# Performance work log

Hardware: AMD Instinct MI355X
Metric: run time of the kernel (lower is better)

## Reference

```python
import jax, jax.numpy as jnp
import numpy as np

HEAD_SIZE = 128
NEG_INF = -1000000000.0

def setup_inputs() -> dict:
    key = jax.random.key(0)
    k1, k2, k3, k4 = jax.random.split(key, 4)
    B, T, C = 8, 2048, 1024
    x = jax.random.normal(k1, (B, T, C), dtype=jnp.float32)
    Wq = jax.random.normal(k2, (C, HEAD_SIZE), dtype=jnp.float32) * (1.0 / np.sqrt(C))
    Wk = jax.random.normal(k3, (C, HEAD_SIZE), dtype=jnp.float32) * (1.0 / np.sqrt(C))
    Wv = jax.random.normal(k4, (C, HEAD_SIZE), dtype=jnp.float32) * (1.0 / np.sqrt(C))
    return {"x": x, "Wq": Wq, "Wk": Wk, "Wv": Wv}

def reference(x, Wq, Wk, Wv):
    # x: [B, T, C]; projections: [B, T, H]
    T = x.shape[1]
    q = jnp.einsum('btc,ch->bth', x, Wq)
    k = jnp.einsum('btc,ch->bth', x, Wk)
    v = jnp.einsum('btc,ch->bth', x, Wv)
    scale = 1.0 / jnp.sqrt(jnp.float32(HEAD_SIZE))
    wei = jnp.einsum('bth,bsh->bts', q, k) * scale  # [B, T, T]
    causal = jnp.tril(jnp.ones((T, T), dtype=bool))
    wei = jnp.where(causal, wei, NEG_INF)
    wei = jax.nn.softmax(wei, axis=-1)
    # dropout is identity (deterministic=True)
    out = jnp.einsum('bts,bsh->bth', wei, v)  # [B, T, H]
    return out
```

## Files before the change

### kernel.cpp

```cpp
#include <hip/hip_runtime.h>
#include <hip/hip_bf16.h>
#include <stdint.h>

#define B_ 8
#define T_ 2048
#define C_ 1024
#define H_ 128
#define BT (B_*T_)
#define SCALE 0.08838834764831845f
#define CH 8

typedef __attribute__((ext_vector_type(8))) short bf16x8;
typedef __attribute__((ext_vector_type(4))) float f32x4;

__device__ __forceinline__ ushort f2bf(float f) {
  union { float f; uint32_t u; } un; un.f = f;
  return (ushort)((un.u + 0x7fffu + ((un.u >> 16) & 1u)) >> 16);
}
__device__ __forceinline__ float bf2f(ushort h) {
  union { uint32_t u; float f; } un; un.u = ((uint32_t)h) << 16;
  return un.f;
}

__global__ __launch_bounds__(256) void wtrans_kernel(
    const float* __restrict__ Wq, const float* __restrict__ Wk,
    const float* __restrict__ Wv, ushort* __restrict__ wt)
{
  const int tt = blockIdx.x * 256 + threadIdx.x;
  const int n = tt >> 6;
  const int k0 = (tt & 63) << 4;
  const float* W = (n < 128) ? Wq : (n < 256 ? Wk : Wv);
  const int h = n & 127;
  ushort tmp[16];
  #pragma unroll
  for (int j = 0; j < 16; ++j)
    tmp[j] = f2bf(W[(size_t)(k0 + j) * H_ + h]);
  *reinterpret_cast<bf16x8*>(&wt[(size_t)n * C_ + k0]) =
      *reinterpret_cast<bf16x8*>(&tmp[0]);
  *reinterpret_cast<bf16x8*>(&wt[(size_t)n * C_ + k0 + 8]) =
      *reinterpret_cast<bf16x8*>(&tmp[8]);
}

__global__ __launch_bounds__(256, 3) void proj_kernel(
    const float* __restrict__ x, const ushort* __restrict__ wt,
    ushort* __restrict__ qh, ushort* __restrict__ kh, ushort* __restrict__ vt)
{
  __shared__ __align__(16) ushort As[64][64];
  __shared__ __align__(16) ushort Bs[128][64];
  const int tid  = threadIdx.x;
  const int lane = tid & 63, wave = tid >> 6;
  const int l15  = lane & 15, l4 = lane >> 4;
  const int o  = (blockIdx.x & 7) * 96 + (blockIdx.x >> 3);
  const int mb = o / 3, nb = o - mb * 3;
  const int m0 = mb * 64, n0 = nb * 128;
  const int wr = wave >> 1, wc = wave & 1;

  f32x4 acc[2][4];
  #pragma unroll
  for (int i = 0; i < 2; ++i)
    #pragma unroll
    for (int j = 0; j < 4; ++j) acc[i][j] = f32x4{0.f, 0.f, 0.f, 0.f};

  for (int k0 = 0; k0 < C_; k0 += 64) {
    __syncthreads();
    #pragma unroll
    for (int it = 0; it < 4; ++it) {
      const int f4 = it * 256 + tid;
      const int r = f4 >> 4, c4 = f4 & 15;
      float4 v = *reinterpret_cast<const float4*>(
          &x[(size_t)(m0 + r) * C_ + k0 + 4 * c4]);
      ushort4 pk;
      pk.x = f2bf(v.x); pk.y = f2bf(v.y); pk.z = f2bf(v.z); pk.w = f2bf(v.w);
      const int ch = (c4 >> 1) ^ (r & 7);
      *reinterpret_cast<ushort4*>(&As[r][ch * 8 + (c4 & 1) * 4]) = pk;
    }
    #pragma unroll
    for (int it = 0; it < 4; ++it) {
      const int f8 = it * 256 + tid;
      const int r = f8 >> 3, c8 = f8 & 7;
      const int ch = c8 ^ (r & 7);
      *reinterpret_cast<bf16x8*>(&Bs[r][ch * 8]) =
          *reinterpret_cast<const bf16x8*>(
              &wt[(size_t)(n0 + r) * C_ + k0 + c8 * 8]);
    }
    __syncthreads();

    bf16x8 a[2][2], b[4][2];
    #pragma unroll
    for (int mi = 0; mi < 2; ++mi)
      #pragma unroll
      for (int kc = 0; kc < 2; ++kc) {
        const int row = wr * 32 + mi * 16 + l15;
        const int ch = (kc * 4 + l4) ^ (row & 7);
        a[mi][kc] = *reinterpret_cast<const bf16x8*>(&As[row][ch * 8]);
      }
    #pragma unroll
    for (int ni = 0; ni < 4; ++ni)
      #pragma unroll
      for (int kc = 0; kc < 2; ++kc) {
        const int row = wc * 64 + ni * 16 + l15;
        const int ch = (kc * 4 + l4) ^ (row & 7);
        b[ni][kc] = *reinterpret_cast<const bf16x8*>(&Bs[row][ch * 8]);
      }

    __builtin_amdgcn_s_setprio(1);
    if (nb != 2) {
      #pragma unroll
      for (int mi = 0; mi < 2; ++mi)
        #pragma unroll
        for (int ni = 0; ni < 4; ++ni)
          #pragma unroll
          for (int kc = 0; kc < 2; ++kc)
            acc[mi][ni] = __builtin_amdgcn_mfma_f32_16x16x32_bf16(
                a[mi][kc], b[ni][kc], acc[mi][ni], 0, 0, 0);
    } else {
      #pragma unroll
      for (int mi = 0; mi < 2; ++mi)
        #pragma unroll
        for (int ni = 0; ni < 4; ++ni)
          #pragma unroll
          for (int kc = 0; kc < 2; ++kc)
            acc[mi][ni] = __builtin_amdgcn_mfma_f32_16x16x32_bf16(
                b[ni][kc], a[mi][kc], acc[mi][ni], 0, 0, 0);
    }
    __builtin_amdgcn_s_setprio(0);
  }

  if (nb != 2) {
    ushort* dst = (nb == 0) ? qh : kh;
    #pragma unroll
    for (int mi = 0; mi < 2; ++mi)
      #pragma unroll
      for (int ni = 0; ni < 4; ++ni)
        #pragma unroll
        for (int reg = 0; reg < 4; ++reg) {
          const int row = m0 + wr * 32 + mi * 16 + l4 * 4 + reg;
          const int col = wc * 64 + ni * 16 + l15;
          dst[(size_t)row * H_ + col] = f2bf(acc[mi][ni][reg]);
        }
  } else {
    #pragma unroll
    for (int mi = 0; mi < 2; ++mi)
      #pragma unroll
      for (int ni = 0; ni < 4; ++ni)
        #pragma unroll
        for (int reg = 0; reg < 4; ++reg) {
          const int h = wc * 64 + ni * 16 + l4 * 4 + reg;
          const int gr = m0 + wr * 32 + mi * 16 + l15;
          const int b = gr >> 11, t = gr & 2047;
          vt[((size_t)b * H_ + h) * T_ + t] = f2bf(acc[mi][ni][reg]);
        }
  }
}

__global__ __launch_bounds__(256) void attn_kernel(
    const ushort* __restrict__ qh, const ushort* __restrict__ kh,
    const ushort* __restrict__ vt, ushort* __restrict__ pO,
    float* __restrict__ pm, float* __restrict__ pl, float* __restrict__ out)
{
  __shared__ __align__(16) ushort Ks[64][128];
  __shared__ __align__(16) ushort Vs[128][64];
  __shared__ __align__(16) ushort Ps[4][16][64];
  const int tid  = threadIdx.x;
  const int lane = tid & 63, wave = tid >> 6;
  const int l15  = lane & 15, l4 = lane >> 4;
  const int o = (blockIdx.x & 7) * 80 + (blockIdx.x >> 3);
  const int b = o / 80, u = o % 80;
  int g = 0;
  if (u >= 8)  g = 1;
  if (u >= 24) g = 2;
  if (u >= 48) g = 3;
  const int gp1 = g + 1;
  const int u2 = u - 4 * g * gp1;
  const int qi = 8 * g + u2 / gp1;
  const int ci = u2 % gp1;
  const int nchunk = gp1;
  const int q0 = qi * 64;
  const int kt0 = ci * CH;
  const int kt1 = min(qi + 1, kt0 + CH);
  const size_t mbase = (size_t)b * T_ + q0;
  const int swz = l15 & 7;

  bf16x8 qa[4];
  {
    const ushort* qrow = &qh[(mbase + wave * 16 + l15) * H_];
    #pragma unroll
    for (int kc = 0; kc < 4; ++kc)
      qa[kc] = *reinterpret_cast<const bf16x8*>(&qrow[kc * 32 + l4 * 8]);
  }

  f32x4 o_[8];
  #pragma unroll
  for (int i = 0; i < 8; ++i) o_[i] = f32x4{0.f, 0.f, 0.f, 0.f};
  float mrow[4] = {-1e9f, -1e9f, -1e9f, -1e9f};
  float lrow[4] = {0.f, 0.f, 0.f, 0.f};

  for (int kt = kt0; kt < kt1; ++kt) {
    const int kv0 = kt * 64;
    __syncthreads();
    for (int i = tid; i < 1024; i += 256) {
      const int r = i >> 4, c8 = i & 15;
      const int c8s = (c8 & 7) ^ (r & 7);
      *reinterpret_cast<bf16x8*>(&Ks[r][((c8 & 8) | c8s) * 8]) =
          *reinterpret_cast<const bf16x8*>(
              &kh[((size_t)b * T_ + kv0 + r) * H_ + c8 * 8]);
    }
    for (int i = tid; i < 1024; i += 256) {
      const int r = i >> 3, c8 = i & 7;
      const int c8s = c8 ^ (r & 7);
      *reinterpret_cast<bf16x8*>(&Vs[r][c8s * 8]) =
          *reinterpret_cast<const bf16x8*>(
              &vt[((size_t)b * H_ + r) * T_ + kv0 + c8 * 8]);
    }
    __syncthreads();

    f32x4 s[4];
    __builtin_amdgcn_s_setprio(1);
    #pragma unroll
    for (int ct = 0; ct < 4; ++ct) {
      s[ct] = f32x4{0.f, 0.f, 0.f, 0.f};
      #pragma unroll
      for (int kc = 0; kc < 4; ++kc) {
        const int chunk = ((kc * 4 + l4) & 7) ^ swz;
        bf16x8 kb = *reinterpret_cast<const bf16x8*>(
            &Ks[ct * 16 + l15][(((kc * 4 + l4) & 8) | chunk) * 8]);
        s[ct] = __builtin_amdgcn_mfma_f32_16x16x32_bf16(qa[kc], kb, s[ct], 0, 0, 0);
      }
    }
    __builtin_amdgcn_s_setprio(0);

    const bool diag = (kv0 == q0);
    float sv[4][4];
    #pragma unroll
    for (int ct = 0; ct < 4; ++ct)
      #pragma unroll
      for (int reg = 0; reg < 4; ++reg) {
        float v = s[ct][reg] * SCALE;
        if (diag) {
          const int sg = kv0 + ct * 16 + l15;
          const int rg = q0 + wave * 16 + l4 * 4 + reg;
          if (sg > rg) v = -1e9f;
        }
        sv[ct][reg] = v;
      }
    float mnew[4], alpha[4], ls[4];
    #pragma unroll
    for (int reg = 0; reg < 4; ++reg) {
      float m = fmaxf(fmaxf(sv[0][reg], sv[1][reg]), fmaxf(sv[2][reg], sv[3][reg]));
      #pragma unroll
      for (int msk = 1; msk < 16; msk <<= 1) m = fmaxf(m, __shfl_xor(m, msk));
      mnew[reg]  = fmaxf(mrow[reg], m);
      alpha[reg] = __expf(mrow[reg] - mnew[reg]);
      ls[reg] = 0.f;
    }
    #pragma unroll
    for (int ct = 0; ct < 4; ++ct)
      #pragma unroll
      for (int reg = 0; reg < 4; ++reg) {
        const float p = __expf(sv[ct][reg] - mnew[reg]);
        ls[reg] += p;
        const int prow = l4 * 4 + reg;
        Ps[wave][prow][(ct * 16 + l15) ^ ((prow & 7) * 8)] = f2bf(p);
      }
    #pragma unroll
    for (int reg = 0; reg < 4; ++reg) {
      float t = ls[reg];
      #pragma unroll
      for (int msk = 1; msk < 16; msk <<= 1) t += __shfl_xor(t, msk);
      lrow[reg] = lrow[reg] * alpha[reg] + t;
      mrow[reg] = mnew[reg];
    }
    #pragma unroll
    for (int ct = 0; ct < 8; ++ct)
      #pragma unroll
      for (int reg = 0; reg < 4; ++reg) o_[ct][reg] *= alpha[reg];
    bf16x8 pa[2];
    #pragma unroll
    for (int kc = 0; kc < 2; ++kc)
      pa[kc] = *reinterpret_cast<const bf16x8*>(
          &Ps[wave][l15][((kc * 4 + l4) ^ swz) * 8]);
    __builtin_amdgcn_s_setprio(1);
    #pragma unroll
    for (int ct = 0; ct < 8; ++ct) {
      #pragma unroll
      for (int kc = 0; kc < 2; ++kc) {
        bf16x8 vb = *reinterpret_cast<const bf16x8*>(
            &Vs[ct * 16 + l15][((kc * 4 + l4) ^ swz) * 8]);
        o_[ct] = __builtin_amdgcn_mfma_f32_16x16x32_bf16(pa[kc], vb, o_[ct], 0, 0, 0);
      }
    }
    __builtin_amdgcn_s_setprio(0);
  }

  if (nchunk == 1) {
    #pragma unroll
    for (int ct = 0; ct < 8; ++ct)
      #pragma unroll
      for (int reg = 0; reg < 4; ++reg) {
        const size_t row = mbase + wave * 16 + l4 * 4 + reg;
        out[row * H_ + ct * 16 + l15] = o_[ct][reg] / lrow[reg];
      }
  } else {
    const size_t slot = ((size_t)(b * 32 + qi)) * 4 + ci;
    ushort* po = pO + slot * 64 * 128;
    #pragma unroll
    for (int ct = 0; ct < 8; ++ct)
      #pragma unroll
      for (int reg = 0; reg < 4; ++reg) {
        const int row = wave * 16 + l4 * 4 + reg;
        po[(size_t)row * 128 + ct * 16 + l15] = f2bf(o_[ct][reg]);
      }
    #pragma unroll
    for (int reg = 0; reg < 4; ++reg) {
      if (l15 == 0) {
        const int row = wave * 16 + l4 * 4 + reg;
        pm[slot * 64 + row] = mrow[reg];
        pl[slot * 64 + row] = lrow[reg];
      }
    }
  }
}

__global__ __launch_bounds__(256) void combine_kernel(
    const ushort* __restrict__ pO, const float* __restrict__ pm,
    const float* __restrict__ pl, float* __restrict__ out)
{
  const int o = blockIdx.x;
  const int b = o / 24, qi = 8 + o % 24;
  const int nc = (qi >> 3) + 1;
  const int tid = threadIdx.x;
  const int row = tid >> 2, cg = tid & 3;
  const size_t slotbase = ((size_t)(b * 32 + qi)) * 4;

  float M = -1e30f;
  for (int ci = 0; ci < nc; ++ci)
    M = fmaxf(M, pm[(slotbase + ci) * 64 + row]);

  float L = 0.f;
  float acc[32];
  #pragma unroll
  for (int j = 0; j < 32; ++j) acc[j] = 0.f;
  for (int ci = 0; ci < nc; ++ci) {
    const float e = __expf(pm[(slotbase + ci) * 64 + row] - M);
    L += pl[(slotbase + ci) * 64 + row] * e;
    const ushort* src = pO + (slotbase + ci) * 8192 + (size_t)row * 128 + cg * 32;
    #pragma unroll
    for (int j4 = 0; j4 < 4; ++j4) {
      bf16x8 v = *reinterpret_cast<const bf16x8*>(&src[j4 * 8]);
      #pragma unroll
      for (int j = 0; j < 8; ++j)
        acc[j4 * 8 + j] += e * bf2f((ushort)v[j]);
    }
  }
  const float inv = 1.f / L;
  float* dst = out + ((size_t)b * T_ + qi * 64 + row) * H_ + cg * 32;
  #pragma unroll
  for (int j4 = 0; j4 < 8; ++j4) {
    float4 w;
    w.x = acc[j4 * 4 + 0] * inv; w.y = acc[j4 * 4 + 1] * inv;
    w.z = acc[j4 * 4 + 2] * inv; w.w = acc[j4 * 4 + 3] * inv;
    *reinterpret_cast<float4*>(&dst[j4 * 4]) = w;
  }
}

extern "C" void kernel_launch(void* const* d_in, const int* in_sizes, int n_in,
                              void* d_out, int out_size, void* d_ws, size_t ws_size,
                              hipStream_t stream) {
  const float* x  = (const float*)d_in[0];
  const float* Wq = (const float*)d_in[1];
  const float* Wk = (const float*)d_in[2];
  const float* Wv = (const float*)d_in[3];
  float* out = (float*)d_out;
  ushort* qh = (ushort*)d_ws;
  ushort* kh = qh + (size_t)BT * H_;
  ushort* vt = kh + (size_t)BT * H_;
  ushort* wt = vt + (size_t)B_ * H_ * T_;
  ushort* pO = wt + (size_t)384 * C_;
  float*  pm = (float*)(pO + (size_t)8 * 32 * 4 * 64 * 128);
  float*  pl = pm + (size_t)8 * 32 * 4 * 64;
  wtrans_kernel<<<96, 256, 0, stream>>>(Wq, Wk, Wv, wt);
  proj_kernel<<<768, 256, 0, stream>>>(x, wt, qh, kh, vt);
  attn_kernel<<<640, 256, 0, stream>>>(qh, kh, vt, pO, pm, pl, out);
  combine_kernel<<<192, 256, 0, stream>>>(pO, pm, pl, out);
}
```

Before: 79.77 us.

## Double-buffer projection GEMM, fold scale into Q, split attention KV chunks finer

The projection kernel now double-buffers its LDS tiles. It prefetches the next K-slice into registers while MFMAs run on the current one, cutting one barrier per iteration. The softmax scale is applied to Q at projection time, which removes a multiply per score in attention. Attention splits KV into chunks of 4 tiles instead of 8, giving 1152 blocks with a new slot layout, which means more partial outputs for the combine kernel to merge.

```diff
diff --git a/kernel.cpp b/kernel.cpp
--- a/kernel.cpp
+++ b/kernel.cpp
@@ -8,7 +8,8 @@
 #define H_ 128
 #define BT (B_*T_)
 #define SCALE 0.08838834764831845f
-#define CH 8
+#define CH 4
+#define SLOTS_PB 140
 
 typedef __attribute__((ext_vector_type(8))) short bf16x8;
 typedef __attribute__((ext_vector_type(4))) float f32x4;
@@ -45,8 +46,8 @@
     const float* __restrict__ x, const ushort* __restrict__ wt,
     ushort* __restrict__ qh, ushort* __restrict__ kh, ushort* __restrict__ vt)
 {
-  __shared__ __align__(16) ushort As[64][64];
-  __shared__ __align__(16) ushort Bs[128][64];
+  __shared__ __align__(16) ushort As[2][64][64];
+  __shared__ __align__(16) ushort Bs[2][128][64];
   const int tid  = threadIdx.x;
   const int lane = tid & 63, wave = tid >> 6;
   const int l15  = lane & 15, l4 = lane >> 4;
@@ -61,29 +62,51 @@
     #pragma unroll
     for (int j = 0; j < 4; ++j) acc[i][j] = f32x4{0.f, 0.f, 0.f, 0.f};
 
-  for (int k0 = 0; k0 < C_; k0 += 64) {
-    __syncthreads();
+  float4 av[4];
+  bf16x8 bv[4];
+  auto issue_loads = [&](int k0) {
     #pragma unroll
     for (int it = 0; it < 4; ++it) {
       const int f4 = it * 256 + tid;
       const int r = f4 >> 4, c4 = f4 & 15;
-      float4 v = *reinterpret_cast<const float4*>(
+      av[it] = *reinterpret_cast<const float4*>(
           &x[(size_t)(m0 + r) * C_ + k0 + 4 * c4]);
+    }
+    #pragma unroll
+    for (int it = 0; it < 4; ++it) {
+      const int f8 = it * 256 + tid;
+      const int r = f8 >> 3, c8 = f8 & 7;
+      bv[it] = *reinterpret_cast<const bf16x8*>(
+          &wt[(size_t)(n0 + r) * C_ + k0 + c8 * 8]);
+    }
+  };
+  auto write_lds = [&](int buf) {
+    #pragma unroll
+    for (int it = 0; it < 4; ++it) {
+      const int f4 = it * 256 + tid;
+      const int r = f4 >> 4, c4 = f4 & 15;
       ushort4 pk;
-      pk.x = f2bf(v.x); pk.y = f2bf(v.y); pk.z = f2bf(v.z); pk.w = f2bf(v.w);
+      pk.x = f2bf(av[it].x); pk.y = f2bf(av[it].y);
+      pk.z = f2bf(av[it].z); pk.w = f2bf(av[it].w);
       const int ch = (c4 >> 1) ^ (r & 7);
-      *reinterpret_cast<ushort4*>(&As[r][ch * 8 + (c4 & 1) * 4]) = pk;
+      *reinterpret_cast<ushort4*>(&As[buf][r][ch * 8 + (c4 & 1) * 4]) = pk;
     }
     #pragma unroll
     for (int it = 0; it < 4; ++it) {
       const int f8 = it * 256 + tid;
       const int r = f8 >> 3, c8 = f8 & 7;
       const int ch = c8 ^ (r & 7);
-      *reinterpret_cast<bf16x8*>(&Bs[r][ch * 8]) =
-          *reinterpret_cast<const bf16x8*>(
-              &wt[(size_t)(n0 + r) * C_ + k0 + c8 * 8]);
-    }
-    __syncthreads();
+      *reinterpret_cast<bf16x8*>(&Bs[buf][r][ch * 8]) = bv[it];
+    }
+  };
+
+  issue_loads(0);
+  write_lds(0);
+  __syncthreads();
+  int cur = 0;
+  for (int t = 0; t < 16; ++t) {
+    const bool last = (t == 15);
+    if (!last) issue_loads((t + 1) * 64);
 
     bf16x8 a[2][2], b[4][2];
     #pragma unroll
@@ -92,7 +115,7 @@
       for (int kc = 0; kc < 2; ++kc) {
         const int row = wr * 32 + mi * 16 + l15;
         const int ch = (kc * 4 + l4) ^ (row & 7);
-        a[mi][kc] = *reinterpret_cast<const bf16x8*>(&As[row][ch * 8]);
+        a[mi][kc] = *reinterpret_cast<const bf16x8*>(&As[cur][row][ch * 8]);
       }
     #pragma unroll
     for (int ni = 0; ni < 4; ++ni)
@@ -100,7 +123,7 @@
       for (int kc = 0; kc < 2; ++kc) {
         const int row = wc * 64 + ni * 16 + l15;
         const int ch = (kc * 4 + l4) ^ (row & 7);
-        b[ni][kc] = *reinterpret_cast<const bf16x8*>(&Bs[row][ch * 8]);
+        b[ni][kc] = *reinterpret_cast<const bf16x8*>(&Bs[cur][row][ch * 8]);
       }
 
     __builtin_amdgcn_s_setprio(1);
@@ -124,10 +147,15 @@
                 b[ni][kc], a[mi][kc], acc[mi][ni], 0, 0, 0);
     }
     __builtin_amdgcn_s_setprio(0);
+
+    if (!last) write_lds(cur ^ 1);
+    __syncthreads();
+    cur ^= 1;
   }
 
   if (nb != 2) {
     ushort* dst = (nb == 0) ? qh : kh;
+    const float mul = (nb == 0) ? SCALE : 1.0f;
     #pragma unroll
     for (int mi = 0; mi < 2; ++mi)
       #pragma unroll
@@ -136,7 +164,7 @@
         for (int reg = 0; reg < 4; ++reg) {
           const int row = m0 + wr * 32 + mi * 16 + l4 * 4 + reg;
           const int col = wc * 64 + ni * 16 + l15;
-          dst[(size_t)row * H_ + col] = f2bf(acc[mi][ni][reg]);
+          dst[(size_t)row * H_ + col] = f2bf(acc[mi][ni][reg] * mul);
         }
   } else {
     #pragma unroll
@@ -164,17 +192,19 @@
   const int tid  = threadIdx.x;
   const int lane = tid & 63, wave = tid >> 6;
   const int l15  = lane & 15, l4 = lane >> 4;
-  const int o = (blockIdx.x & 7) * 80 + (blockIdx.x >> 3);
-  const int b = o / 80, u = o % 80;
-  int g = 0;
-  if (u >= 8)  g = 1;
-  if (u >= 24) g = 2;
-  if (u >= 48) g = 3;
-  const int gp1 = g + 1;
-  const int u2 = u - 4 * g * gp1;
-  const int qi = 8 * g + u2 / gp1;
-  const int ci = u2 % gp1;
-  const int nchunk = gp1;
+  const int o = (blockIdx.x & 7) * 144 + (blockIdx.x >> 3);
+  const int b = o / 144;
+  const int u = o - b * 144;
+  int qi, ci, nchunk, u2 = 0;
+  if (u < 4) { qi = u; ci = 0; nchunk = 1; }
+  else {
+    u2 = u - 4;
+    int rem = u2, g = 1;
+    while (rem >= 4 * (g + 1)) { rem -= 4 * (g + 1); ++g; }
+    nchunk = g + 1;
+    qi = 4 * g + rem / nchunk;
+    ci = rem - (rem / nchunk) * nchunk;
+  }
   const int q0 = qi * 64;
   const int kt0 = ci * CH;
   const int kt1 = min(qi + 1, kt0 + CH);
@@ -235,7 +265,7 @@
     for (int ct = 0; ct < 4; ++ct)
       #pragma unroll
       for (int reg = 0; reg < 4; ++reg) {
-        float v = s[ct][reg] * SCALE;
+        float v = s[ct][reg];
         if (diag) {
           const int sg = kv0 + ct * 16 + l15;
           const int rg = q0 + wave * 16 + l4 * 4 + reg;
@@ -301,7 +331,7 @@
         out[row * H_ + ct * 16 + l15] = o_[ct][reg] / lrow[reg];
       }
   } else {
-    const size_t slot = ((size_t)(b * 32 + qi)) * 4 + ci;
+    const size_t slot = (size_t)b * SLOTS_PB + u2;
     ushort* po = pO + slot * 64 * 128;
     #pragma unroll
     for (int ct = 0; ct < 8; ++ct)
@@ -326,11 +356,13 @@
     const float* __restrict__ pl, float* __restrict__ out)
 {
   const int o = blockIdx.x;
-  const int b = o / 24, qi = 8 + o % 24;
-  const int nc = (qi >> 3) + 1;
+  const int b = o / 28, qi = 4 + o % 28;
+  const int G = qi >> 2;
+  const int nc = G + 1;
   const int tid = threadIdx.x;
   const int row = tid >> 2, cg = tid & 3;
-  const size_t slotbase = ((size_t)(b * 32 + qi)) * 4;
+  const size_t slotbase =
+      (size_t)b * SLOTS_PB + 2 * (G - 1) * (G + 2) + (qi & 3) * (G + 1);
 
   float M = -1e30f;
   for (int ci = 0; ci < nc; ++ci)
@@ -376,10 +408,10 @@
   ushort* vt = kh + (size_t)BT * H_;
   ushort* wt = vt + (size_t)B_ * H_ * T_;
   ushort* pO = wt + (size_t)384 * C_;
-  float*  pm = (float*)(pO + (size_t)8 * 32 * 4 * 64 * 128);
-  float*  pl = pm + (size_t)8 * 32 * 4 * 64;
+  float*  pm = (float*)(pO + (size_t)B_ * SLOTS_PB * 64 * 128);
+  float*  pl = pm + (size_t)B_ * SLOTS_PB * 64;
   wtrans_kernel<<<96, 256, 0, stream>>>(Wq, Wk, Wv, wt);
   proj_kernel<<<768, 256, 0, stream>>>(x, wt, qh, kh, vt);
-  attn_kernel<<<640, 256, 0, stream>>>(qh, kh, vt, pO, pm, pl, out);
-  combine_kernel<<<192, 256, 0, stream>>>(pO, pm, pl, out);
-}
+  attn_kernel<<<1152, 256, 0, stream>>>(qh, kh, vt, pO, pm, pl, out);
+  combine_kernel<<<224, 256, 0, stream>>>(pO, pm, pl, out);
+}
```

New measurement: 100.6 us. +26.1%, slower.
